# Kernel tuning notes

Hardware: AMD Instinct MI355X
Metric: run time of the kernel (lower is better)

The kernel has to match this reference:

```python
import jax, jax.numpy as jnp
import numpy as np

N_NODES = 100000
HIDDEN = 256
HALF = HIDDEN // 2
N_EDGES = 1000000


def setup_inputs() -> dict:
    key = jax.random.key(0)
    k1, k2 = jax.random.split(key)
    x = jax.random.normal(k1, (N_NODES, HIDDEN), dtype=jnp.float32)
    edge_label_index = jax.random.randint(k2, (2, N_EDGES), 0, N_NODES, dtype=jnp.int64)
    return {"x": x, "edge_label_index": edge_label_index}


def reference(x, edge_label_index):
    # Gather source-half features for src nodes and target-half for dst nodes,
    # per-edge dot product, sigmoid. Output shape [E, 1] as in the torch module.
    src = x[edge_label_index[0], :HALF]          # [E, HALF]
    dst = x[edge_label_index[1], HALF:]          # [E, HALF]
    logits = jnp.einsum('ed,ed->e', src, dst)    # per-edge dot
    return jax.nn.sigmoid(logits).reshape(-1, 1)
```

## Files before the change

kernel.cpp:

```cpp
#include <hip/hip_runtime.h>
#include <hip/hip_bf16.h>
#include <math.h>


#define HIDDEN 256
#define HALF   128

typedef _Float16 half8 __attribute__((ext_vector_type(8)));

__global__ __launch_bounds__(256) void cvt_fp16_kernel(
    const float* __restrict__ x, _Float16* __restrict__ y, int n8)
{
    int i = blockIdx.x * blockDim.x + threadIdx.x;
    if (i >= n8) return;
    const float4* p = (const float4*)x + (size_t)2 * i;
    float4 a = p[0];
    float4 b = p[1];
    half8 h;
    h[0] = (_Float16)a.x; h[1] = (_Float16)a.y;
    h[2] = (_Float16)a.z; h[3] = (_Float16)a.w;
    h[4] = (_Float16)b.x; h[5] = (_Float16)b.y;
    h[6] = (_Float16)b.z; h[7] = (_Float16)b.w;
    ((half8*)y)[i] = h;
}

__global__ __launch_bounds__(256) void decoder_fp16_kernel(
    const _Float16* __restrict__ y,
    const int* __restrict__ eidx,
    float* __restrict__ out,
    int n_edges)
{
    int tid  = blockIdx.x * blockDim.x + threadIdx.x;
    int edge = tid >> 4;
    int lane = tid & 15;
    if (edge >= n_edges) return;

    int s = eidx[edge];
    int d = eidx[n_edges + edge];

    const half8* sp = (const half8*)(y + (size_t)s * HIDDEN) + lane;
    const half8* dp = (const half8*)(y + (size_t)d * HIDDEN + HALF) + lane;

    half8 a = *sp;
    half8 b = *dp;

    float acc = 0.f;
    #pragma unroll
    for (int j = 0; j < 8; ++j)
        acc += (float)a[j] * (float)b[j];

    #pragma unroll
    for (int off = 8; off > 0; off >>= 1)
        acc += __shfl_down(acc, off, 16);

    if (lane == 0) {
        out[edge] = 1.0f / (1.0f + __expf(-acc));
    }
}

__global__ __launch_bounds__(256) void decoder_fp32_kernel(
    const float* __restrict__ x,
    const int* __restrict__ eidx,
    float* __restrict__ out,
    int n_edges)
{
    int tid  = blockIdx.x * blockDim.x + threadIdx.x;
    int edge = tid >> 5;
    int lane = tid & 31;
    if (edge >= n_edges) return;

    int s = eidx[edge];
    int d = eidx[n_edges + edge];

    const float4* sp = (const float4*)(x + (size_t)s * HIDDEN) + lane;
    const float4* dp = (const float4*)(x + (size_t)d * HIDDEN + HALF) + lane;

    float4 a = *sp;
    float4 b = *dp;
    float acc = a.x * b.x + a.y * b.y + a.z * b.z + a.w * b.w;

    #pragma unroll
    for (int off = 16; off > 0; off >>= 1)
        acc += __shfl_down(acc, off, 32);

    if (lane == 0) {
        out[edge] = 1.0f / (1.0f + __expf(-acc));
    }
}

extern "C" void kernel_launch(void* const* d_in, const int* in_sizes, int n_in,
                              void* d_out, int out_size, void* d_ws, size_t ws_size,
                              hipStream_t stream)
{
    const float* x    = (const float*)d_in[0];
    const int*   eidx = (const int*)d_in[1];
    float*       out  = (float*)d_out;

    int n_edges  = out_size;
    int n_elems  = in_sizes[0];
    size_t need  = (size_t)n_elems * 2;

    if (ws_size >= need) {
        _Float16* y = (_Float16*)d_ws;

        int n8 = n_elems / 8;
        cvt_fp16_kernel<<<(n8 + 255) / 256, 256, 0, stream>>>(x, y, n8);

        const int threads = 256;
        const int epb = threads / 16;
        int blocks = (n_edges + epb - 1) / epb;
        decoder_fp16_kernel<<<blocks, threads, 0, stream>>>(y, eidx, out, n_edges);
    } else {
        const int threads = 256;
        const int epb = threads / 32;
        int blocks = (n_edges + epb - 1) / epb;
        decoder_fp32_kernel<<<blocks, threads, 0, stream>>>(x, eidx, out, n_edges);
    }
}
```

Measured before the change: 225.0 us.

## Batch four edges per 16-lane group, use fdot2, and unroll fp16 conversion

The decoder now has each 16-lane group handle four edges. It loads the indices as int4, issues eight independent row gathers, reduces them with fdot2 and four interleaved shuffle reductions, and writes a float4 of sigmoids. The fp32-to-fp16 conversion kernel now uses a grid-strided layout where each thread loads eight float4s before converting, to raise memory-level parallelism. This adds a divisibility requirement on the element count for the fp16 path and raises register pressure per thread.

```diff
diff --git a/kernel.cpp b/kernel.cpp
--- a/kernel.cpp
+++ b/kernel.cpp
@@ -7,21 +7,48 @@
 #define HALF   128
 
 typedef _Float16 half8 __attribute__((ext_vector_type(8)));
+typedef _Float16 half4 __attribute__((ext_vector_type(4)));
+typedef _Float16 half2_t __attribute__((ext_vector_type(2)));
+
+#define CVT_ITER 8
 
 __global__ __launch_bounds__(256) void cvt_fp16_kernel(
-    const float* __restrict__ x, _Float16* __restrict__ y, int n8)
+    const float* __restrict__ x, _Float16* __restrict__ y, int n4)
 {
-    int i = blockIdx.x * blockDim.x + threadIdx.x;
-    if (i >= n8) return;
-    const float4* p = (const float4*)x + (size_t)2 * i;
-    float4 a = p[0];
-    float4 b = p[1];
-    half8 h;
-    h[0] = (_Float16)a.x; h[1] = (_Float16)a.y;
-    h[2] = (_Float16)a.z; h[3] = (_Float16)a.w;
-    h[4] = (_Float16)b.x; h[5] = (_Float16)b.y;
-    h[6] = (_Float16)b.z; h[7] = (_Float16)b.w;
-    ((half8*)y)[i] = h;
+    int t = blockIdx.x * blockDim.x + threadIdx.x;
+    int stride = gridDim.x * blockDim.x;
+
+    const float4* x4 = (const float4*)x;
+    half4* y4 = (half4*)y;
+
+    float4 v[CVT_ITER];
+    int idx[CVT_ITER];
+    #pragma unroll
+    for (int k = 0; k < CVT_ITER; ++k) {
+        idx[k] = t + k * stride;
+        v[k] = x4[idx[k]];
+    }
+    #pragma unroll
+    for (int k = 0; k < CVT_ITER; ++k) {
+        half4 h;
+        h[0] = (_Float16)v[k].x;
+        h[1] = (_Float16)v[k].y;
+        h[2] = (_Float16)v[k].z;
+        h[3] = (_Float16)v[k].w;
+        y4[idx[k]] = h;
+    }
+}
+
+__device__ __forceinline__ float dot8(half8 a, half8 b)
+{
+    float acc = 0.f;
+    #pragma unroll
+    for (int j = 0; j < 4; ++j) {
+        half2_t aj = { a[2*j], a[2*j+1] };
+        half2_t bj = { b[2*j], b[2*j+1] };
+        acc = __builtin_amdgcn_fdot2(aj, bj, acc, false);
+    }
+    return acc;
 }
 
 __global__ __launch_bounds__(256) void decoder_fp16_kernel(
@@ -30,31 +57,60 @@
     float* __restrict__ out,
     int n_edges)
 {
-    int tid  = blockIdx.x * blockDim.x + threadIdx.x;
-    int edge = tid >> 4;
-    int lane = tid & 15;
-    if (edge >= n_edges) return;
+    int tid   = blockIdx.x * blockDim.x + threadIdx.x;
+    int group = tid >> 4;
+    int lane  = tid & 15;
+    int e0 = group << 2;
+    if (e0 >= n_edges) return;
+    bool full = (e0 + 3) < n_edges;
 
-    int s = eidx[edge];
-    int d = eidx[n_edges + edge];
+    int4 se, de;
+    if (full) {
+        se = *(const int4*)(eidx + e0);
+        de = *(const int4*)(eidx + n_edges + e0);
+    } else {
+        int s = eidx[e0], d = eidx[n_edges + e0];
+        se = make_int4(s, s, s, s);
+        de = make_int4(d, d, d, d);
+        if (e0 + 1 < n_edges) { se.y = eidx[e0+1]; de.y = eidx[n_edges+e0+1]; }
+        if (e0 + 2 < n_edges) { se.z = eidx[e0+2]; de.z = eidx[n_edges+e0+2]; }
+    }
 
-    const half8* sp = (const half8*)(y + (size_t)s * HIDDEN) + lane;
-    const half8* dp = (const half8*)(y + (size_t)d * HIDDEN + HALF) + lane;
+    half8 a0 = ((const half8*)(y + (size_t)se.x * HIDDEN))[lane];
+    half8 b0 = ((const half8*)(y + (size_t)de.x * HIDDEN + HALF))[lane];
+    half8 a1 = ((const half8*)(y + (size_t)se.y * HIDDEN))[lane];
+    half8 b1 = ((const half8*)(y + (size_t)de.y * HIDDEN + HALF))[lane];
+    half8 a2 = ((const half8*)(y + (size_t)se.z * HIDDEN))[lane];
+    half8 b2 = ((const half8*)(y + (size_t)de.z * HIDDEN + HALF))[lane];
+    half8 a3 = ((const half8*)(y + (size_t)se.w * HIDDEN))[lane];
+    half8 b3 = ((const half8*)(y + (size_t)de.w * HIDDEN + HALF))[lane];
 
-    half8 a = *sp;
-    half8 b = *dp;
-
-    float acc = 0.f;
-    #pragma unroll
-    for (int j = 0; j < 8; ++j)
-        acc += (float)a[j] * (float)b[j];
+    float acc0 = dot8(a0, b0);
+    float acc1 = dot8(a1, b1);
+    float acc2 = dot8(a2, b2);
+    float acc3 = dot8(a3, b3);
 
     #pragma unroll
-    for (int off = 8; off > 0; off >>= 1)
-        acc += __shfl_down(acc, off, 16);
+    for (int off = 8; off > 0; off >>= 1) {
+        acc0 += __shfl_down(acc0, off, 16);
+        acc1 += __shfl_down(acc1, off, 16);
+        acc2 += __shfl_down(acc2, off, 16);
+        acc3 += __shfl_down(acc3, off, 16);
+    }
 
     if (lane == 0) {
-        out[edge] = 1.0f / (1.0f + __expf(-acc));
+        float4 r;
+        r.x = 1.0f / (1.0f + __expf(-acc0));
+        r.y = 1.0f / (1.0f + __expf(-acc1));
+        r.z = 1.0f / (1.0f + __expf(-acc2));
+        r.w = 1.0f / (1.0f + __expf(-acc3));
+        if (full) {
+            ((float4*)out)[group] = r;
+        } else {
+            out[e0] = r.x;
+            if (e0 + 1 < n_edges) out[e0+1] = r.y;
+            if (e0 + 2 < n_edges) out[e0+2] = r.z;
+        }
     }
 }
 
@@ -100,15 +156,17 @@
     int n_elems  = in_sizes[0];
     size_t need  = (size_t)n_elems * 2;
 
-    if (ws_size >= need) {
+    if (ws_size >= need && (n_elems % (256 * CVT_ITER * 4)) == 0) {
         _Float16* y = (_Float16*)d_ws;
 
-        int n8 = n_elems / 8;
-        cvt_fp16_kernel<<<(n8 + 255) / 256, 256, 0, stream>>>(x, y, n8);
+        int n4 = n_elems / 4;
+        int threads_total = n4 / CVT_ITER;
+        cvt_fp16_kernel<<<threads_total / 256, 256, 0, stream>>>(x, y, n4);
 
         const int threads = 256;
-        const int epb = threads / 16;
-        int blocks = (n_edges + epb - 1) / epb;
+        int groups = (n_edges + 3) / 4;
+        long long total = (long long)groups * 16;
+        int blocks = (int)((total + threads - 1) / threads);
         decoder_fp16_kernel<<<blocks, threads, 0, stream>>>(y, eidx, out, n_edges);
     } else {
         const int threads = 256;
```

Measured after the change: 224.6 us. Within noise of the previous version (-0.2%).
